# Optimization experiments

Measured on AMD Instinct MI355X. Metric: run time of the kernel, lower is better.

The kernel has to match this reference:

```python
import jax, jax.numpy as jnp
import numpy as np

EPS = 1e-12  # matches tf.nn.l2_normalize epsilon used by keras backend


def l2n(x, axis):
    return x / jnp.sqrt(jnp.maximum(jnp.sum(x * x, axis=axis, keepdims=True), EPS))


def setup_inputs() -> dict:
    key = jax.random.key(0)
    k1, k2, k3 = jax.random.split(key, 3)
    B, T, D, P = 32, 256, 512, 20
    inp_a = jax.random.normal(k1, (B, T, D), dtype=jnp.float32)
    inp_b = jax.random.normal(k2, (B, T, D), dtype=jnp.float32)
    # build(): output_dim weights of shape (1, D), 'uniform' init -> stacked (P, D)
    W = jax.random.uniform(k3, (P, D), dtype=jnp.float32, minval=-0.05, maxval=0.05)
    return {"inp_a": inp_a, "inp_b": inp_b, "W": W}


def reference(inp_a, inp_b, W):
    # l2-normalize over feature dim
    na = l2n(inp_a, -1)  # (B,T,D)
    nb = l2n(inp_b, -1)  # (B,T,D)
    # K.batch_dot(outp_b, outp_a, axes=[1,1]): contract seq axis -> (B,D,D)
    alpha = jnp.einsum('btd,bte->bde', nb, na)
    alpha = l2n(alpha, 1)
    # K.batch_dot(outp_b, alpha, axes=[2,1]): contract feature axis of b with axis1 of alpha -> (B,T,D)
    hmean = jnp.einsum('btd,bde->bte', nb, alpha)
    # per-perspective weighting + l2-normalize, vectorized over P perspectives
    aw = l2n(inp_a[:, :, None, :] * W[None, None, :, :], -1)   # (B,T,P,D)
    hw = l2n(hmean[:, :, None, :] * W[None, None, :, :], -1)   # (B,T,P,D)
    # batch_dot(hw_i, aw_i, axes=[2,2]) * eye summed == rowwise dot (diagonal only)
    persp = jnp.sum(aw * hw, axis=-1)  # (B,T,P)
    return (persp, persp)
```

## Files before the change

### kernel.cpp

```cpp
#include <hip/hip_runtime.h>
#include <hip/hip_bf16.h>

#define BB 32
#define TT 256
#define DD 512
#define PP 20
#define EPSF 1e-12f
#define BTP (BB * TT * PP)

typedef __attribute__((ext_vector_type(8))) short short8;
typedef __attribute__((ext_vector_type(4))) float f32x4;

__device__ inline unsigned short f2bf(float f) {
    unsigned u = __float_as_uint(f);
    u += 0x7fffu + ((u >> 16) & 1u);
    return (unsigned short)(u >> 16);
}
__device__ inline unsigned pk2(float lo, float hi) {
    __hip_bfloat162 h = __float22bfloat162_rn(float2{lo, hi});
    union { __hip_bfloat162 h; unsigned u; } c;
    c.h = h;
    return c.u;
}
__device__ inline float bf2f(unsigned s) {
    return __uint_as_float(s << 16);
}

union U8 { short8 s; uint4 u; };

__global__ __launch_bounds__(256)
void k_prep(const float* __restrict__ a, const float* __restrict__ b,
            const float* __restrict__ W,
            unsigned short* __restrict__ na_bf,
            unsigned short* __restrict__ nb_bf,
            float* __restrict__ q, unsigned short* __restrict__ W2) {
    const int row  = blockIdx.x * 4 + (threadIdx.x >> 6);
    const int lane = threadIdx.x & 63;
    const float4* pa = (const float4*)(a + (size_t)row * DD);
    const float4* pb = (const float4*)(b + (size_t)row * DD);
    float4 a0 = pa[2 * lane], a1 = pa[2 * lane + 1];
    float4 b0 = pb[2 * lane], b1 = pb[2 * lane + 1];
    float sa = a0.x * a0.x + a0.y * a0.y + a0.z * a0.z + a0.w * a0.w
             + a1.x * a1.x + a1.y * a1.y + a1.z * a1.z + a1.w * a1.w;
    float sb = b0.x * b0.x + b0.y * b0.y + b0.z * b0.z + b0.w * b0.w
             + b1.x * b1.x + b1.y * b1.y + b1.z * b1.z + b1.w * b1.w;
#pragma unroll
    for (int off = 1; off < 64; off <<= 1) {
        sa += __shfl_xor(sa, off);
        sb += __shfl_xor(sb, off);
    }
    const float ia_ = rsqrtf(fmaxf(sa, EPSF));
    const float ib_ = rsqrtf(fmaxf(sb, EPSF));
    uint4 oa, ob;
    oa.x = pk2(a0.x * ia_, a0.y * ia_);
    oa.y = pk2(a0.z * ia_, a0.w * ia_);
    oa.z = pk2(a1.x * ia_, a1.y * ia_);
    oa.w = pk2(a1.z * ia_, a1.w * ia_);
    ob.x = pk2(b0.x * ib_, b0.y * ib_);
    ob.y = pk2(b0.z * ib_, b0.w * ib_);
    ob.z = pk2(b1.x * ib_, b1.y * ib_);
    ob.w = pk2(b1.z * ib_, b1.w * ib_);
    *(uint4*)(na_bf + (size_t)row * DD + 8 * lane) = oa;
    *(uint4*)(nb_bf + (size_t)row * DD + 8 * lane) = ob;
    if (lane < 2) {
        const int i2 = 2 * row + lane;
        q[i2] = 0.f;
        const float w = (i2 < PP * DD) ? W[i2] : 0.f;
        W2[i2] = f2bf(w * w);
    }
}

__global__ __launch_bounds__(256)
void k_gemm_g(const unsigned short* __restrict__ nb,
              unsigned short* __restrict__ G) {
    const int bz  = blockIdx.z;
    const int tid = threadIdx.x;
    const int t0 = blockIdx.y * 64;
    const int s0 = blockIdx.x * 64;
    __shared__ __align__(16) unsigned short As[64 * 40];
    __shared__ __align__(16) unsigned short Bs[64 * 40];

    const int wave = tid >> 6, lane = tid & 63;
    const int quad = lane >> 4, ln = lane & 15;
    const int wm = wave >> 1, wn = wave & 1;

    const unsigned short* nbb = nb + (size_t)bz * TT * DD;

    const int lr = tid >> 2;
    const int c8 = (tid & 3) * 8;

    f32x4 acc[2][2];
#pragma unroll
    for (int i = 0; i < 2; ++i)
#pragma unroll
        for (int j = 0; j < 2; ++j)
#pragma unroll
            for (int r = 0; r < 4; ++r) acc[i][j][r] = 0.f;

    for (int k0 = 0; k0 < DD; k0 += 32) {
        *(uint4*)&As[lr * 40 + c8] =
            *(const uint4*)(nbb + (size_t)(t0 + lr) * DD + k0 + c8);
        *(uint4*)&Bs[lr * 40 + c8] =
            *(const uint4*)(nbb + (size_t)(s0 + lr) * DD + k0 + c8);
        __syncthreads();
        short8 af[2], bf[2];
        af[0] = *(const short8*)&As[(wm * 32 + ln) * 40 + quad * 8];
        af[1] = *(const short8*)&As[(wm * 32 + 16 + ln) * 40 + quad * 8];
        bf[0] = *(const short8*)&Bs[(wn * 32 + ln) * 40 + quad * 8];
        bf[1] = *(const short8*)&Bs[(wn * 32 + 16 + ln) * 40 + quad * 8];
#pragma unroll
        for (int i = 0; i < 2; ++i)
#pragma unroll
            for (int j = 0; j < 2; ++j)
                acc[i][j] = __builtin_amdgcn_mfma_f32_16x16x32_bf16(
                    af[i], bf[j], acc[i][j], 0, 0, 0);
        __syncthreads();
    }
    unsigned short* Gb = G + (size_t)bz * TT * TT;
#pragma unroll
    for (int i = 0; i < 2; ++i)
#pragma unroll
        for (int j = 0; j < 2; ++j) {
            const int col = s0 + wn * 32 + j * 16 + ln;
            const int row0 = t0 + wm * 32 + i * 16 + quad * 4;
#pragma unroll
            for (int r = 0; r < 4; r += 2) {
                const unsigned pk = pk2(acc[i][j][r], acc[i][j][r + 1]);
                Gb[(size_t)(row0 + r) * TT + col] = (unsigned short)pk;
                Gb[(size_t)(row0 + r + 1) * TT + col] = (unsigned short)(pk >> 16);
            }
        }
}

__global__ __launch_bounds__(256)
void k_gemm_h(const unsigned short* __restrict__ G,
              const unsigned short* __restrict__ na,
              unsigned short* __restrict__ H, float* __restrict__ q) {
    const int bz = blockIdx.z;
    const int t0 = blockIdx.y * 64;
    const int e0 = blockIdx.x * 64;
    __shared__ __align__(16) unsigned short As[64 * 40];
    __shared__ __align__(16) unsigned short Bs[64 * 40];
    __shared__ float qsum[64];

    const int tid  = threadIdx.x;
    const int wave = tid >> 6, lane = tid & 63;
    const int quad = lane >> 4, ln = lane & 15;
    const int wm = wave >> 1, wn = wave & 1;

    const unsigned short* Gb  = G  + (size_t)bz * TT * TT;
    const unsigned short* nab = na + (size_t)bz * TT * DD;

    const int lr = tid >> 2;
    const int c8 = (tid & 3) * 8;
    const int kr = tid >> 3;
    const int e8 = (tid & 7) * 8;

    f32x4 acc[2][2];
#pragma unroll
    for (int i = 0; i < 2; ++i)
#pragma unroll
        for (int j = 0; j < 2; ++j)
#pragma unroll
            for (int r = 0; r < 4; ++r) acc[i][j][r] = 0.f;

    for (int k0 = 0; k0 < TT; k0 += 32) {
        *(uint4*)&As[lr * 40 + c8] =
            *(const uint4*)(Gb + (size_t)(t0 + lr) * TT + k0 + c8);
        {
            uint4 v = *(const uint4*)(nab + (size_t)(k0 + kr) * DD + e0 + e8);
            Bs[(e8 + 0) * 40 + kr] = (unsigned short)(v.x);
            Bs[(e8 + 1) * 40 + kr] = (unsigned short)(v.x >> 16);
            Bs[(e8 + 2) * 40 + kr] = (unsigned short)(v.y);
            Bs[(e8 + 3) * 40 + kr] = (unsigned short)(v.y >> 16);
            Bs[(e8 + 4) * 40 + kr] = (unsigned short)(v.z);
            Bs[(e8 + 5) * 40 + kr] = (unsigned short)(v.z >> 16);
            Bs[(e8 + 6) * 40 + kr] = (unsigned short)(v.w);
            Bs[(e8 + 7) * 40 + kr] = (unsigned short)(v.w >> 16);
        }
        __syncthreads();
        short8 af[2], bf[2];
        af[0] = *(const short8*)&As[(wm * 32 + ln) * 40 + quad * 8];
        af[1] = *(const short8*)&As[(wm * 32 + 16 + ln) * 40 + quad * 8];
        bf[0] = *(const short8*)&Bs[(wn * 32 + ln) * 40 + quad * 8];
        bf[1] = *(const short8*)&Bs[(wn * 32 + 16 + ln) * 40 + quad * 8];
#pragma unroll
        for (int i = 0; i < 2; ++i)
#pragma unroll
            for (int j = 0; j < 2; ++j)
                acc[i][j] = __builtin_amdgcn_mfma_f32_16x16x32_bf16(
                    af[i], bf[j], acc[i][j], 0, 0, 0);
        __syncthreads();
    }

    if (tid < 64) qsum[tid] = 0.f;
    __syncthreads();

    unsigned short* Hb = H + (size_t)bz * TT * DD;
#pragma unroll
    for (int j = 0; j < 2; ++j) {
        const int col = e0 + wn * 32 + j * 16 + ln;
        float qp = 0.f;
#pragma unroll
        for (int i = 0; i < 2; ++i) {
            const int row0 = t0 + wm * 32 + i * 16 + quad * 4;
#pragma unroll
            for (int r = 0; r < 4; r += 2) {
                const float hv0 = acc[i][j][r];
                const float hv1 = acc[i][j][r + 1];
                const unsigned pk = pk2(hv0, hv1);
                Hb[(size_t)(row0 + r) * DD + col] = (unsigned short)pk;
                Hb[(size_t)(row0 + r + 1) * DD + col] = (unsigned short)(pk >> 16);
                qp = fmaf(bf2f(nab[(size_t)(row0 + r) * DD + col]), hv0, qp);
                qp = fmaf(bf2f(nab[(size_t)(row0 + r + 1) * DD + col]), hv1, qp);
            }
        }
        qp += __shfl_xor(qp, 16);
        qp += __shfl_xor(qp, 32);
        if (quad == 0) atomicAdd(&qsum[wn * 32 + j * 16 + ln], qp);
    }
    __syncthreads();
    if (tid < 64) atomicAdd(q + bz * DD + e0 + tid, qsum[tid]);
}

__global__ __launch_bounds__(128)
void k_persp_mfma(const unsigned short* __restrict__ na,
                  const unsigned short* __restrict__ H,
                  const float* __restrict__ q,
                  const unsigned short* __restrict__ W2,
                  float* __restrict__ out) {
    const int b    = blockIdx.y;
    const int r0   = blockIdx.x * 16;
    const int wave = threadIdx.x >> 6;
    const int lane = threadIdx.x & 63;
    const int quad = lane >> 4, ln = lane & 15;
    const size_t rowbase = ((size_t)b * TT + r0 + ln) * DD;

    __shared__ float qs[DD];
    __shared__ float ps[64][24];
    {
        const float* qb = q + (size_t)b * DD;
        float4 v = *(const float4*)(qb + 4 * threadIdx.x);
        qs[4 * threadIdx.x + 0] = rsqrtf(fmaxf(v.x, EPSF));
        qs[4 * threadIdx.x + 1] = rsqrtf(fmaxf(v.y, EPSF));
        qs[4 * threadIdx.x + 2] = rsqrtf(fmaxf(v.z, EPSF));
        qs[4 * threadIdx.x + 3] = rsqrtf(fmaxf(v.w, EPSF));
    }
    __syncthreads();

    f32x4 s1[2], s2[2], s3[2];
#pragma unroll
    for (int j = 0; j < 2; ++j)
#pragma unroll
        for (int r = 0; r < 4; ++r) { s1[j][r] = 0.f; s2[j][r] = 0.f; s3[j][r] = 0.f; }

    const int kbeg = wave * 256;
    for (int k0 = kbeg; k0 < kbeg + 256; k0 += 32) {
        const int k = k0 + quad * 8;
        uint4 au = *(const uint4*)(na + rowbase + k);
        uint4 hu = *(const uint4*)(H + rowbase + k);
        float4 q0 = *(const float4*)&qs[k];
        float4 q1 = *(const float4*)&qs[k + 4];
        const float av[8] = {bf2f(au.x & 0xffffu), bf2f(au.x >> 16),
                             bf2f(au.y & 0xffffu), bf2f(au.y >> 16),
                             bf2f(au.z & 0xffffu), bf2f(au.z >> 16),
                             bf2f(au.w & 0xffffu), bf2f(au.w >> 16)};
        const float qv[8] = {q0.x, q0.y, q0.z, q0.w, q1.x, q1.y, q1.z, q1.w};
        float hv[8] = {bf2f(hu.x & 0xffffu), bf2f(hu.x >> 16),
                       bf2f(hu.y & 0xffffu), bf2f(hu.y >> 16),
                       bf2f(hu.z & 0xffffu), bf2f(hu.z >> 16),
                       bf2f(hu.w & 0xffffu), bf2f(hu.w >> 16)};
#pragma unroll
        for (int t = 0; t < 8; ++t) hv[t] *= qv[t];
        U8 ah, aa, hh;
        ah.u.x = pk2(av[0] * hv[0], av[1] * hv[1]);
        ah.u.y = pk2(av[2] * hv[2], av[3] * hv[3]);
        ah.u.z = pk2(av[4] * hv[4], av[5] * hv[5]);
        ah.u.w = pk2(av[6] * hv[6], av[7] * hv[7]);
        aa.u.x = pk2(av[0] * av[0], av[1] * av[1]);
        aa.u.y = pk2(av[2] * av[2], av[3] * av[3]);
        aa.u.z = pk2(av[4] * av[4], av[5] * av[5]);
        aa.u.w = pk2(av[6] * av[6], av[7] * av[7]);
        hh.u.x = pk2(hv[0] * hv[0], hv[1] * hv[1]);
        hh.u.y = pk2(hv[2] * hv[2], hv[3] * hv[3]);
        hh.u.z = pk2(hv[4] * hv[4], hv[5] * hv[5]);
        hh.u.w = pk2(hv[6] * hv[6], hv[7] * hv[7]);
        short8 bw0 = *(const short8*)(W2 + (size_t)ln * DD + k);
        short8 bw1 = *(const short8*)(W2 + (size_t)(16 + ln) * DD + k);
        s1[0] = __builtin_amdgcn_mfma_f32_16x16x32_bf16(ah.s, bw0, s1[0], 0, 0, 0);
        s1[1] = __builtin_amdgcn_mfma_f32_16x16x32_bf16(ah.s, bw1, s1[1], 0, 0, 0);
        s2[0] = __builtin_amdgcn_mfma_f32_16x16x32_bf16(aa.s, bw0, s2[0], 0, 0, 0);
        s2[1] = __builtin_amdgcn_mfma_f32_16x16x32_bf16(aa.s, bw1, s2[1], 0, 0, 0);
        s3[0] = __builtin_amdgcn_mfma_f32_16x16x32_bf16(hh.s, bw0, s3[0], 0, 0, 0);
        s3[1] = __builtin_amdgcn_mfma_f32_16x16x32_bf16(hh.s, bw1, s3[1], 0, 0, 0);
    }

    if (wave == 1) {
#pragma unroll
        for (int j = 0; j < 2; ++j)
#pragma unroll
            for (int r = 0; r < 4; ++r) {
                ps[lane][j * 4 + r]      = s1[j][r];
                ps[lane][8 + j * 4 + r]  = s2[j][r];
                ps[lane][16 + j * 4 + r] = s3[j][r];
            }
    }
    __syncthreads();
    if (wave == 0) {
#pragma unroll
        for (int j = 0; j < 2; ++j) {
            const int p = j * 16 + ln;
            if (p < PP) {
#pragma unroll
                for (int r = 0; r < 4; ++r) {
                    const float v1 = s1[j][r] + ps[lane][j * 4 + r];
                    const float v2 = s2[j][r] + ps[lane][8 + j * 4 + r];
                    const float v3 = s3[j][r] + ps[lane][16 + j * 4 + r];
                    const size_t row = (size_t)b * TT + r0 + quad * 4 + r;
                    const float v = v1 * rsqrtf(fmaxf(v2, EPSF))
                                       * rsqrtf(fmaxf(v3, EPSF));
                    out[row * PP + p] = v;
                    out[(size_t)BTP + row * PP + p] = v;
                }
            }
        }
    }
}

extern "C" void kernel_launch(void* const* d_in, const int* in_sizes, int n_in,
                              void* d_out, int out_size, void* d_ws, size_t ws_size,
                              hipStream_t stream) {
    (void)in_sizes; (void)n_in; (void)out_size; (void)ws_size;
    const float* a = (const float*)d_in[0];
    const float* b = (const float*)d_in[1];
    const float* W = (const float*)d_in[2];
    float* out = (float*)d_out;

    char* ws = (char*)d_ws;
    unsigned short* nb_bf = (unsigned short*)ws;
    unsigned short* na_bf = (unsigned short*)(ws + (8u << 20));
    unsigned short* G_bf  = (unsigned short*)(ws + (16u << 20));
    unsigned short* H_bf  = (unsigned short*)(ws + (20u << 20));
    float* q     = (float*)(ws + (28u << 20));
    unsigned short* W2 = (unsigned short*)(ws + (28u << 20) + (64u << 10));

    k_prep<<<BB * TT / 4, 256, 0, stream>>>(a, b, W, na_bf, nb_bf, q, W2);

    dim3 gG(4, 4, BB);
    k_gemm_g<<<gG, 256, 0, stream>>>(nb_bf, G_bf);

    dim3 gH(DD / 64, TT / 64, BB);
    k_gemm_h<<<gH, 256, 0, stream>>>(G_bf, na_bf, H_bf, q);

    dim3 gP(TT / 16, BB);
    k_persp_mfma<<<gP, 128, 0, stream>>>(na_bf, H_bf, q, W2, out);
}
```

Measured before the change: 110.2 us.

## Prefetch GEMM tiles into registers, pack transposed stores, widen perspective kernel

The G GEMM now uses a 64-wide K step and register-prefetches the next tile while the current one is consumed. The H GEMM also register-prefetches. It replaces its eight scalar 16-bit transposed LDS stores per thread with 32-bit packed stores built from two source rows, done by half the threads. The perspective kernel moves from 2 to 4 waves per block, splitting the D reduction four ways and combining the partials through a larger shared buffer. These changes aim to hide global load latency and cut LDS store traffic, at the cost of more registers and shared memory.

```diff
diff --git a/kernel.cpp b/kernel.cpp
--- a/kernel.cpp
+++ b/kernel.cpp
@@ -77,8 +77,8 @@
     const int tid = threadIdx.x;
     const int t0 = blockIdx.y * 64;
     const int s0 = blockIdx.x * 64;
-    __shared__ __align__(16) unsigned short As[64 * 40];
-    __shared__ __align__(16) unsigned short Bs[64 * 40];
+    __shared__ __align__(16) unsigned short As[64 * 72];
+    __shared__ __align__(16) unsigned short Bs[64 * 72];
 
     const int wave = tid >> 6, lane = tid & 63;
     const int quad = lane >> 4, ln = lane & 15;
@@ -86,8 +86,8 @@
 
     const unsigned short* nbb = nb + (size_t)bz * TT * DD;
 
-    const int lr = tid >> 2;
-    const int c8 = (tid & 3) * 8;
+    const int lr  = tid >> 2;
+    const int c16 = (tid & 3) * 16;
 
     f32x4 acc[2][2];
 #pragma unroll
@@ -97,23 +97,39 @@
 #pragma unroll
             for (int r = 0; r < 4; ++r) acc[i][j][r] = 0.f;
 
-    for (int k0 = 0; k0 < DD; k0 += 32) {
-        *(uint4*)&As[lr * 40 + c8] =
-            *(const uint4*)(nbb + (size_t)(t0 + lr) * DD + k0 + c8);
-        *(uint4*)&Bs[lr * 40 + c8] =
-            *(const uint4*)(nbb + (size_t)(s0 + lr) * DD + k0 + c8);
+    uint4 pa0 = *(const uint4*)(nbb + (size_t)(t0 + lr) * DD + c16);
+    uint4 pa1 = *(const uint4*)(nbb + (size_t)(t0 + lr) * DD + c16 + 8);
+    uint4 pb0 = *(const uint4*)(nbb + (size_t)(s0 + lr) * DD + c16);
+    uint4 pb1 = *(const uint4*)(nbb + (size_t)(s0 + lr) * DD + c16 + 8);
+
+    for (int k0 = 0; k0 < DD; k0 += 64) {
+        *(uint4*)&As[lr * 72 + c16]     = pa0;
+        *(uint4*)&As[lr * 72 + c16 + 8] = pa1;
+        *(uint4*)&Bs[lr * 72 + c16]     = pb0;
+        *(uint4*)&Bs[lr * 72 + c16 + 8] = pb1;
+        if (k0 + 64 < DD) {
+            pa0 = *(const uint4*)(nbb + (size_t)(t0 + lr) * DD + k0 + 64 + c16);
+            pa1 = *(const uint4*)(nbb + (size_t)(t0 + lr) * DD + k0 + 64 + c16 + 8);
+            pb0 = *(const uint4*)(nbb + (size_t)(s0 + lr) * DD + k0 + 64 + c16);
+            pb1 = *(const uint4*)(nbb + (size_t)(s0 + lr) * DD + k0 + 64 + c16 + 8);
+        }
         __syncthreads();
-        short8 af[2], bf[2];
-        af[0] = *(const short8*)&As[(wm * 32 + ln) * 40 + quad * 8];
-        af[1] = *(const short8*)&As[(wm * 32 + 16 + ln) * 40 + quad * 8];
-        bf[0] = *(const short8*)&Bs[(wn * 32 + ln) * 40 + quad * 8];
-        bf[1] = *(const short8*)&Bs[(wn * 32 + 16 + ln) * 40 + quad * 8];
-#pragma unroll
-        for (int i = 0; i < 2; ++i)
-#pragma unroll
-            for (int j = 0; j < 2; ++j)
-                acc[i][j] = __builtin_amdgcn_mfma_f32_16x16x32_bf16(
-                    af[i], bf[j], acc[i][j], 0, 0, 0);
+        short8 af[2][2], bfr[2][2];
+#pragma unroll
+        for (int h = 0; h < 2; ++h) {
+            af[h][0]  = *(const short8*)&As[(wm * 32 + ln) * 72 + h * 32 + quad * 8];
+            af[h][1]  = *(const short8*)&As[(wm * 32 + 16 + ln) * 72 + h * 32 + quad * 8];
+            bfr[h][0] = *(const short8*)&Bs[(wn * 32 + ln) * 72 + h * 32 + quad * 8];
+            bfr[h][1] = *(const short8*)&Bs[(wn * 32 + 16 + ln) * 72 + h * 32 + quad * 8];
+        }
+#pragma unroll
+        for (int h = 0; h < 2; ++h)
+#pragma unroll
+            for (int i = 0; i < 2; ++i)
+#pragma unroll
+                for (int j = 0; j < 2; ++j)
+                    acc[i][j] = __builtin_amdgcn_mfma_f32_16x16x32_bf16(
+                        af[h][i], bfr[h][j], acc[i][j], 0, 0, 0);
         __syncthreads();
     }
     unsigned short* Gb = G + (size_t)bz * TT * TT;
@@ -153,8 +169,9 @@
 
     const int lr = tid >> 2;
     const int c8 = (tid & 3) * 8;
-    const int kr = tid >> 3;
-    const int e8 = (tid & 7) * 8;
+    const int eglow = tid & 3;
+    const int spair = (tid >> 2) & 15;
+    const int eg    = eglow + 4 * (tid >> 6);
 
     f32x4 acc[2][2];
 #pragma unroll
@@ -164,32 +181,51 @@
 #pragma unroll
             for (int r = 0; r < 4; ++r) acc[i][j][r] = 0.f;
 
+    uint4 pga = *(const uint4*)(Gb + (size_t)(t0 + lr) * TT + c8);
+    uint4 cva, cvb;
+    if (tid < 128) {
+        cva = *(const uint4*)(nab + (size_t)(2 * spair) * DD + e0 + eg * 8);
+        cvb = *(const uint4*)(nab + (size_t)(2 * spair + 1) * DD + e0 + eg * 8);
+    }
+
+    unsigned* bp = (unsigned*)Bs;
     for (int k0 = 0; k0 < TT; k0 += 32) {
-        *(uint4*)&As[lr * 40 + c8] =
-            *(const uint4*)(Gb + (size_t)(t0 + lr) * TT + k0 + c8);
-        {
-            uint4 v = *(const uint4*)(nab + (size_t)(k0 + kr) * DD + e0 + e8);
-            Bs[(e8 + 0) * 40 + kr] = (unsigned short)(v.x);
-            Bs[(e8 + 1) * 40 + kr] = (unsigned short)(v.x >> 16);
-            Bs[(e8 + 2) * 40 + kr] = (unsigned short)(v.y);
-            Bs[(e8 + 3) * 40 + kr] = (unsigned short)(v.y >> 16);
-            Bs[(e8 + 4) * 40 + kr] = (unsigned short)(v.z);
-            Bs[(e8 + 5) * 40 + kr] = (unsigned short)(v.z >> 16);
-            Bs[(e8 + 6) * 40 + kr] = (unsigned short)(v.w);
-            Bs[(e8 + 7) * 40 + kr] = (unsigned short)(v.w >> 16);
+        *(uint4*)&As[lr * 40 + c8] = pga;
+        if (tid < 128) {
+            const int base = eg * 160 + spair;
+            unsigned lo, hi;
+            lo = cva.x; hi = cvb.x;
+            bp[base +   0] = (lo & 0xffffu) | (hi << 16);
+            bp[base +  20] = (lo >> 16) | (hi & 0xffff0000u);
+            lo = cva.y; hi = cvb.y;
+            bp[base +  40] = (lo & 0xffffu) | (hi << 16);
+            bp[base +  60] = (lo >> 16) | (hi & 0xffff0000u);
+            lo = cva.z; hi = cvb.z;
+            bp[base +  80] = (lo & 0xffffu) | (hi << 16);
+            bp[base + 100] = (lo >> 16) | (hi & 0xffff0000u);
+            lo = cva.w; hi = cvb.w;
+            bp[base + 120] = (lo & 0xffffu) | (hi << 16);
+            bp[base + 140] = (lo >> 16) | (hi & 0xffff0000u);
+        }
+        if (k0 + 32 < TT) {
+            pga = *(const uint4*)(Gb + (size_t)(t0 + lr) * TT + k0 + 32 + c8);
+            if (tid < 128) {
+                cva = *(const uint4*)(nab + (size_t)(k0 + 32 + 2 * spair) * DD + e0 + eg * 8);
+                cvb = *(const uint4*)(nab + (size_t)(k0 + 32 + 2 * spair + 1) * DD + e0 + eg * 8);
+            }
         }
         __syncthreads();
-        short8 af[2], bf[2];
-        af[0] = *(const short8*)&As[(wm * 32 + ln) * 40 + quad * 8];
-        af[1] = *(const short8*)&As[(wm * 32 + 16 + ln) * 40 + quad * 8];
-        bf[0] = *(const short8*)&Bs[(wn * 32 + ln) * 40 + quad * 8];
-        bf[1] = *(const short8*)&Bs[(wn * 32 + 16 + ln) * 40 + quad * 8];
+        short8 af[2], bfr[2];
+        af[0]  = *(const short8*)&As[(wm * 32 + ln) * 40 + quad * 8];
+        af[1]  = *(const short8*)&As[(wm * 32 + 16 + ln) * 40 + quad * 8];
+        bfr[0] = *(const short8*)&Bs[(wn * 32 + ln) * 40 + quad * 8];
+        bfr[1] = *(const short8*)&Bs[(wn * 32 + 16 + ln) * 40 + quad * 8];
 #pragma unroll
         for (int i = 0; i < 2; ++i)
 #pragma unroll
             for (int j = 0; j < 2; ++j)
                 acc[i][j] = __builtin_amdgcn_mfma_f32_16x16x32_bf16(
-                    af[i], bf[j], acc[i][j], 0, 0, 0);
+                    af[i], bfr[j], acc[i][j], 0, 0, 0);
         __syncthreads();
     }
 
@@ -223,7 +259,7 @@
     if (tid < 64) atomicAdd(q + bz * DD + e0 + tid, qsum[tid]);
 }
 
-__global__ __launch_bounds__(128)
+__global__ __launch_bounds__(256)
 void k_persp_mfma(const unsigned short* __restrict__ na,
                   const unsigned short* __restrict__ H,
                   const float* __restrict__ q,
@@ -237,14 +273,12 @@
     const size_t rowbase = ((size_t)b * TT + r0 + ln) * DD;
 
     __shared__ float qs[DD];
-    __shared__ float ps[64][24];
+    __shared__ float ps[3][64][24];
     {
         const float* qb = q + (size_t)b * DD;
-        float4 v = *(const float4*)(qb + 4 * threadIdx.x);
-        qs[4 * threadIdx.x + 0] = rsqrtf(fmaxf(v.x, EPSF));
-        qs[4 * threadIdx.x + 1] = rsqrtf(fmaxf(v.y, EPSF));
-        qs[4 * threadIdx.x + 2] = rsqrtf(fmaxf(v.z, EPSF));
-        qs[4 * threadIdx.x + 3] = rsqrtf(fmaxf(v.w, EPSF));
+        float2 v = *(const float2*)(qb + 2 * threadIdx.x);
+        qs[2 * threadIdx.x + 0] = rsqrtf(fmaxf(v.x, EPSF));
+        qs[2 * threadIdx.x + 1] = rsqrtf(fmaxf(v.y, EPSF));
     }
     __syncthreads();
 
@@ -254,8 +288,8 @@
 #pragma unroll
         for (int r = 0; r < 4; ++r) { s1[j][r] = 0.f; s2[j][r] = 0.f; s3[j][r] = 0.f; }
 
-    const int kbeg = wave * 256;
-    for (int k0 = kbeg; k0 < kbeg + 256; k0 += 32) {
+    const int kbeg = wave * 128;
+    for (int k0 = kbeg; k0 < kbeg + 128; k0 += 32) {
         const int k = k0 + quad * 8;
         uint4 au = *(const uint4*)(na + rowbase + k);
         uint4 hu = *(const uint4*)(H + rowbase + k);
@@ -295,14 +329,14 @@
         s3[1] = __builtin_amdgcn_mfma_f32_16x16x32_bf16(hh.s, bw1, s3[1], 0, 0, 0);
     }
 
-    if (wave == 1) {
+    if (wave >= 1) {
 #pragma unroll
         for (int j = 0; j < 2; ++j)
 #pragma unroll
             for (int r = 0; r < 4; ++r) {
-                ps[lane][j * 4 + r]      = s1[j][r];
-                ps[lane][8 + j * 4 + r]  = s2[j][r];
-                ps[lane][16 + j * 4 + r] = s3[j][r];
+                ps[wave - 1][lane][j * 4 + r]      = s1[j][r];
+                ps[wave - 1][lane][8 + j * 4 + r]  = s2[j][r];
+                ps[wave - 1][lane][16 + j * 4 + r] = s3[j][r];
             }
     }
     __syncthreads();
@@ -313,9 +347,12 @@
             if (p < PP) {
 #pragma unroll
                 for (int r = 0; r < 4; ++r) {
-                    const float v1 = s1[j][r] + ps[lane][j * 4 + r];
-                    const float v2 = s2[j][r] + ps[lane][8 + j * 4 + r];
-                    const float v3 = s3[j][r] + ps[lane][16 + j * 4 + r];
+                    const float v1 = s1[j][r] + ps[0][lane][j * 4 + r]
+                                   + ps[1][lane][j * 4 + r] + ps[2][lane][j * 4 + r];
+                    const float v2 = s2[j][r] + ps[0][lane][8 + j * 4 + r]
+                                   + ps[1][lane][8 + j * 4 + r] + ps[2][lane][8 + j * 4 + r];
+                    const float v3 = s3[j][r] + ps[0][lane][16 + j * 4 + r]
+                                   + ps[1][lane][16 + j * 4 + r] + ps[2][lane][16 + j * 4 + r];
                     const size_t row = (size_t)b * TT + r0 + quad * 4 + r;
                     const float v = v1 * rsqrtf(fmaxf(v2, EPSF))
                                        * rsqrtf(fmaxf(v3, EPSF));
@@ -353,5 +390,5 @@
     k_gemm_h<<<gH, 256, 0, stream>>>(G_bf, na_bf, H_bf, q);
 
     dim3 gP(TT / 16, BB);
-    k_persp_mfma<<<gP, 128, 0, stream>>>(na_bf, H_bf, q, W2, out);
-}
+    k_persp_mfma<<<gP, 256, 0, stream>>>(na_bf, H_bf, q, W2, out);
+}
```

New measurement: 105.7 us. -4.1%, faster.
